# Kernel optimization log

Measured on AMD Instinct MI355X. Metric: run time of the kernel, lower is better.

## Reference

```python
import jax, jax.numpy as jnp
import numpy as np
import math

N = 20000      # nodes
E = 150000     # edges
IN = 256       # in_dim
HID = 256      # n_hid / out_dim
T = 4          # num_types
R = 8          # num_relations
H = 8          # n_heads
DK = HID // H  # d_k = 32
L = 2          # n_layers
MAXLEN = 240   # RTE max_len


def _rte_table():
    # fixed sinusoid table from RelTemporalEncoding (requires_grad=False in torch)
    pos = np.arange(MAXLEN, dtype=np.float64)[:, None]
    div = np.exp(np.arange(0, HID, 2, dtype=np.float64) * -(math.log(10000.0) / HID))
    emb = np.zeros((MAXLEN, HID), dtype=np.float64)
    emb[:, 0::2] = np.sin(pos * div) / math.sqrt(HID)
    emb[:, 1::2] = np.cos(pos * div) / math.sqrt(HID)
    return jnp.asarray(emb, dtype=jnp.float32)


def setup_inputs() -> dict:
    key = jax.random.key(0)
    ks = jax.random.split(key, 20)
    node_feature = jax.random.normal(ks[0], (N, IN), jnp.float32)
    node_type = jax.random.randint(ks[1], (N,), 0, T)
    edge_index = jax.random.randint(ks[2], (2, E), 0, N)
    edge_type = jax.random.randint(ks[3], (E,), 0, R)
    edge_time = jax.random.randint(ks[4], (E,), 0, MAXLEN)

    s_in = 1.0 / math.sqrt(IN)
    s_h = 1.0 / math.sqrt(HID)
    s_g = math.sqrt(2.0 / (DK + DK))  # glorot for relation mats

    adapt_W = jax.random.normal(ks[5], (T, IN, HID), jnp.float32) * s_in
    adapt_b = jnp.zeros((T, HID), jnp.float32)
    k_W = jax.random.normal(ks[6], (L, T, HID, HID), jnp.float32) * s_h
    k_b = jnp.zeros((L, T, HID), jnp.float32)
    q_W = jax.random.normal(ks[7], (L, T, HID, HID), jnp.float32) * s_h
    q_b = jnp.zeros((L, T, HID), jnp.float32)
    v_W = jax.random.normal(ks[8], (L, T, HID, HID), jnp.float32) * s_h
    v_b = jnp.zeros((L, T, HID), jnp.float32)
    a_W = jax.random.normal(ks[9], (L, T, HID, HID), jnp.float32) * s_h
    a_b = jnp.zeros((L, T, HID), jnp.float32)
    rel_pri = jnp.ones((L, R, H), jnp.float32)
    rel_att = jax.random.normal(ks[10], (L, R, H, DK, DK), jnp.float32) * s_g
    rel_msg = jax.random.normal(ks[11], (L, R, H, DK, DK), jnp.float32) * s_g
    skip = jnp.ones((L, T), jnp.float32)
    rte_W = jax.random.normal(ks[12], (L, HID, HID), jnp.float32) * s_h
    rte_b = jnp.zeros((L, HID), jnp.float32)
    rte_emb = _rte_table()

    return dict(node_feature=node_feature, node_type=node_type, edge_time=edge_time,
                edge_index=edge_index, edge_type=edge_type,
                adapt_W=adapt_W, adapt_b=adapt_b, k_W=k_W, k_b=k_b, q_W=q_W, q_b=q_b,
                v_W=v_W, v_b=v_b, a_W=a_W, a_b=a_b, rel_pri=rel_pri, rel_att=rel_att,
                rel_msg=rel_msg, skip=skip, rte_W=rte_W, rte_b=rte_b, rte_emb=rte_emb)


def _typed_linear(x, W, b, types):
    # x: [M, din]; W: [T, din, dout]; per-row type-selected linear (T dense GEMMs + select)
    out = jnp.zeros((x.shape[0], W.shape[-1]), x.dtype)
    for t in range(T):
        out = jnp.where((types == t)[:, None], x @ W[t] + b[t], out)
    return out


def _hgt_forward(node_feature, node_type, edge_time, edge_index, edge_type,
                 adapt_W, adapt_b, k_W, k_b, q_W, q_b, v_W, v_b, a_W, a_b,
                 rel_pri, rel_att, rel_msg, skip, rte_W, rte_b, rte_emb):
    # adapt: per-type tanh(Linear) (dropout is identity at p=0)
    x = jnp.tanh(_typed_linear(node_feature, adapt_W, adapt_b, node_type))
    src, tgt = edge_index[0], edge_index[1]   # j (source), i (target)
    st, tt = node_type[src], node_type[tgt]
    sqrt_dk = math.sqrt(DK)
    att = None
    rte = rte_emb[edge_time]                  # [E, HID]
    for l in range(L):
        x_j = x[src] + (rte @ rte_W[l] + rte_b[l])   # RTE added to source repr
        x_i = x[tgt]
        q = _typed_linear(x_i, q_W[l], q_b[l], tt).reshape(E, H, DK)
        k = _typed_linear(x_j, k_W[l], k_b[l], st).reshape(E, H, DK)
        v = _typed_linear(x_j, v_W[l], v_b[l], st).reshape(E, H, DK)
        att_e = jnp.zeros((E, H), x.dtype)
        msg = jnp.zeros((E, H, DK), x.dtype)
        for r in range(R):
            kr = jnp.einsum('ehd,hdk->ehk', k, rel_att[l, r])
            vr = jnp.einsum('ehd,hdk->ehk', v, rel_msg[l, r])
            a = (q * kr).sum(-1) * rel_pri[l, r] / sqrt_dk
            m = edge_type == r
            att_e = jnp.where(m[:, None], a, att_e)
            msg = jnp.where(m[:, None, None], vr, msg)
        # segment softmax over target node ids
        amax = jax.ops.segment_max(att_e, tgt, num_segments=N)
        ex = jnp.exp(att_e - amax[tgt])
        denom = jax.ops.segment_sum(ex, tgt, num_segments=N)
        alpha = ex / denom[tgt]                       # [E, H]
        agg = jax.ops.segment_sum(msg * alpha[:, :, None], tgt, num_segments=N)
        agg = jax.nn.gelu(agg.reshape(N, HID), approximate=False)
        trans = _typed_linear(agg, a_W[l], a_b[l], node_type)
        sk = jax.nn.sigmoid(skip[l])[node_type][:, None]
        x = trans * sk + x * (1.0 - sk)               # no LayerNorm (use_norm=False)
        att = alpha
    return att, x


def reference(node_feature, node_type, edge_time, edge_index, edge_type,
              adapt_W, adapt_b, k_W, k_b, q_W, q_b, v_W, v_b, a_W, a_b,
              rel_pri, rel_att, rel_msg, skip, rte_W, rte_b, rte_emb):
    return _hgt_forward(node_feature, node_type, edge_time, edge_index, edge_type,
                        adapt_W, adapt_b, k_W, k_b, q_W, q_b, v_W, v_b, a_W, a_b,
                        rel_pri, rel_att, rel_msg, skip, rte_W, rte_b, rte_emb)
```

## Files before the change

### kernel.cpp

```cpp
#include <hip/hip_runtime.h>
#include <hip/hip_fp16.h>

#define NN    20000
#define NE    150000
#define HD    256
#define NT    4
#define NR    8
#define NH    8
#define DKq   32
#define NL    2
#define MAXL  240
#define HBLK  256
#define SCB   ((NN + 255)/256)
#define TMAX  632
#define FOLDN 79
#define FOLDC 15
#define INV_SQRT_DK 0.17677669529663687f

typedef _Float16 f16x4 __attribute__((ext_vector_type(4)));
typedef float    f32x4v __attribute__((ext_vector_type(4)));

__global__ __launch_bounds__(256) void k_nhist(const int* __restrict__ ntype, int* __restrict__ nhist)
{
    __shared__ int h[NT];
    const int tid = threadIdx.x, b = blockIdx.x;
    if (tid < NT) h[tid] = 0;
    __syncthreads();
    const int cn = (NN + HBLK-1)/HBLK;
    const int nEnd = min((b+1)*cn, NN);
    for (int i = b*cn + tid; i < nEnd; i += 256) atomicAdd(&h[ntype[i]], 1);
    __syncthreads();
    if (tid < NT) nhist[b*NT + tid] = h[tid];
}
__global__ void k_nscan(const int* __restrict__ nhist, int* __restrict__ noff, int* __restrict__ nbase,
                        int* __restrict__ tlist, int* __restrict__ tcount)
{
    __shared__ int tot[NT];
    const int tid = threadIdx.x;
    if (tid < NT){
        int s = 0;
        for (int b = 0; b < HBLK; b++) s += nhist[b*NT + tid];
        tot[tid] = s;
    }
    __syncthreads();
    if (tid == 0){ noff[0]=0; for (int t=0;t<NT;t++) noff[t+1]=noff[t]+tot[t]; }
    if (tid < NT){
        int base = 0; for (int t=0;t<tid;t++) base += tot[t];
        int run = 0;
        for (int b=0;b<HBLK;b++){ nbase[b*NT+tid] = base + run; run += nhist[b*NT+tid]; }
    }
    __syncthreads();
    if (tid == 0){
        int c = 0;
        for (int t = 0; t < NT; t++){
            const int ntile = (tot[t] + 31) >> 5;
            for (int rt = 0; rt < ntile; rt++) tlist[c++] = (t << 20) | rt;
        }
        *tcount = c;
    }
}
__global__ __launch_bounds__(256) void k_nscatter(const int* __restrict__ ntype,
    const int* __restrict__ nbase, int* __restrict__ nbucket)
{
    __shared__ int cur[NT];
    const int tid = threadIdx.x, b = blockIdx.x;
    if (tid < NT) cur[tid] = nbase[b*NT + tid];
    __syncthreads();
    const int cn = (NN + HBLK-1)/HBLK;
    const int nEnd = min((b+1)*cn, NN);
    for (int i = b*cn + tid; i < nEnd; i += 256)
        nbucket[atomicAdd(&cur[ntype[i]], 1)] = i;
}

__global__ void k_zero_bins(int* __restrict__ cnt){
    int i = blockIdx.x*256 + threadIdx.x;
    if (i < NN) cnt[i] = 0;
}
__global__ void k_csr_hist(const int* __restrict__ ei, int* __restrict__ cnt){
    int e = blockIdx.x*256 + threadIdx.x;
    if (e >= NE) return;
    atomicAdd(&cnt[ei[NE+e]], 1);
}
__global__ __launch_bounds__(256) void k_scan1(const int* __restrict__ cnt,
    int* __restrict__ tgt_off, int* __restrict__ bsum)
{
    __shared__ int sh[256];
    const int t = threadIdx.x, b = blockIdx.x;
    const int i = b*256 + t;
    const int v = (i < NN) ? cnt[i] : 0;
    sh[t] = v;
    __syncthreads();
    #pragma unroll
    for (int d = 1; d < 256; d <<= 1){
        const int u = (t >= d) ? sh[t-d] : 0;
        __syncthreads();
        sh[t] += u;
        __syncthreads();
    }
    if (i < NN) tgt_off[i] = sh[t] - v;
    if (t == 255) bsum[b] = sh[255];
}
__global__ __launch_bounds__(128) void k_scan2(const int* __restrict__ bsum,
    int* __restrict__ bbase, int* __restrict__ tgt_off)
{
    __shared__ int sh[128];
    const int t = threadIdx.x;
    const int v = (t < SCB) ? bsum[t] : 0;
    sh[t] = v;
    __syncthreads();
    #pragma unroll
    for (int d = 1; d < 128; d <<= 1){
        const int u = (t >= d) ? sh[t-d] : 0;
        __syncthreads();
        sh[t] += u;
        __syncthreads();
    }
    if (t < SCB) bbase[t] = sh[t] - v;
    if (t == 0) tgt_off[NN] = NE;
}
__global__ __launch_bounds__(256) void k_scan3(int* __restrict__ tgt_off,
    const int* __restrict__ bbase, int* __restrict__ binCur)
{
    const int i = blockIdx.x*256 + threadIdx.x;
    if (i >= NN) return;
    const int o = tgt_off[i] + bbase[blockIdx.x];
    tgt_off[i] = o;
    binCur[i] = o;
}
__global__ void k_csr_scatter(const int* __restrict__ ei, const int* __restrict__ etype,
    const int* __restrict__ etime, const int* __restrict__ ntype,
    int* __restrict__ binCur, int* __restrict__ src_s, int* __restrict__ combo_s,
    int* __restrict__ eid_s)
{
    int e = blockIdx.x*256 + threadIdx.x;
    if (e >= NE) return;
    const int tgt = ei[NE+e], r = etype[e], src = ei[e];
    const int pos = atomicAdd(&binCur[tgt], 1);
    src_s[pos] = src;
    combo_s[pos] = (etime[e]*NT + ntype[src]) | (r << 12);
    eid_s[pos] = e;
}
__global__ void k_tgtmap(const int* __restrict__ tgt_off, int* __restrict__ tgt_srt)
{
    const int n = blockIdx.x*256 + threadIdx.x;
    if (n >= NN) return;
    const int e0 = tgt_off[n], e1 = tgt_off[n+1];
    for (int j = e0; j < e1; j++) tgt_srt[j] = n;
}

__global__ __launch_bounds__(256) void k_w2f16_big(
    const float* __restrict__ adaptW, const float* __restrict__ qW, const float* __restrict__ kW,
    const float* __restrict__ vW, const float* __restrict__ aW, _Float16* __restrict__ out)
{
    const int y = blockIdx.y;
    const float* src; int m;
    if (y < 4){ src = adaptW; m = y; }
    else if (y < 12){ src = qW; m = y-4; }
    else if (y < 20){ src = kW; m = y-12; }
    else if (y < 28){ src = vW; m = y-20; }
    else { src = aW; m = y-28; }
    const float* ip = src + (size_t)m*65536;
    _Float16* op = out + (size_t)y*65536;
    const int tid4 = blockIdx.x*256 + threadIdx.x;
    const int k4 = tid4 >> 8, c = tid4 & 255;
    f16x4 hv;
    #pragma unroll
    for (int j = 0; j < 4; j++)
        hv[j] = (_Float16)ip[(size_t)(((k4*4 + j) << 8) + c)];
    *reinterpret_cast<f16x4*>(&op[(size_t)tid4 * 4]) = hv;
}
__global__ __launch_bounds__(256) void k_w2f16_rel(
    const float* __restrict__ attW, const float* __restrict__ msgW, _Float16* __restrict__ out)
{
    const int y = blockIdx.y;
    const float* ip = (y < 128) ? (attW + (size_t)y*1024) : (msgW + (size_t)(y-128)*1024);
    _Float16* op = out + (size_t)y*1024;
    const int tid4 = threadIdx.x;
    const int k4 = tid4 >> 5, c = tid4 & 31;
    f16x4 hv;
    #pragma unroll
    for (int j = 0; j < 4; j++)
        hv[j] = (_Float16)ip[(size_t)(((k4*4 + j) << 5) + c)];
    *reinterpret_cast<f16x4*>(&op[(size_t)tid4 * 4]) = hv;
}

__global__ __launch_bounds__(256) void k_x(
    const float* __restrict__ inF, const _Float16* __restrict__ inH,
    const _Float16* __restrict__ Wb, const float* __restrict__ bb, void* __restrict__ out,
    const int* __restrict__ nbucket, const int* __restrict__ noff,
    const int* __restrict__ tlist, const int* __restrict__ tcount,
    int mode, int oh, const float* __restrict__ skipv, const _Float16* __restrict__ xoldH)
{
    if ((int)blockIdx.x >= *tcount) return;
    const int ent = tlist[blockIdx.x];
    const int t = ent >> 20, rowTile = ent & 0xFFFFF;
    const int start = noff[t], cnt = noff[t+1] - start;

    const int tid = threadIdx.x;
    const int w = tid >> 6, lane = tid & 63;
    const int lrow = lane & 15, lgrp = lane >> 4;

    __shared__ _Float16 Al[32][260];
    __shared__ int nid[32];

    if (tid < 32){
        const int gr = rowTile*32 + tid;
        nid[tid] = (gr < cnt) ? nbucket[start + gr] : -1;
    }
    __syncthreads();
    {
        const int r = tid >> 3;
        const int arow = nid[r];
        if (inH){
            const _Float16* ap = (arow >= 0) ? (inH + (size_t)arow*HD) : nullptr;
            #pragma unroll
            for (int j = 0; j < 8; j++){
                const int f4 = (tid & 7) + j*8;
                f16x4 hv = {0,0,0,0};
                if (ap) hv = *reinterpret_cast<const f16x4*>(ap + f4*4);
                *reinterpret_cast<f16x4*>(&Al[r][f4*4]) = hv;
            }
        } else {
            const float* ap = (arow >= 0) ? (inF + (size_t)arow*HD) : nullptr;
            #pragma unroll
            for (int j = 0; j < 8; j++){
                const int f4 = (tid & 7) + j*8;
                float4 v = make_float4(0.f,0.f,0.f,0.f);
                if (ap) v = *reinterpret_cast<const float4*>(ap + f4*4);
                f16x4 hv;
                hv[0]=(_Float16)v.x; hv[1]=(_Float16)v.y; hv[2]=(_Float16)v.z; hv[3]=(_Float16)v.w;
                *reinterpret_cast<f16x4*>(&Al[r][f4*4]) = hv;
            }
        }
    }
    __syncthreads();

    float sk = 0.f;
    if (mode == 2) sk = 1.f/(1.f + __expf(-skipv[t]));

    const _Float16* W = Wb + (size_t)t*HD*HD;
    const float* bias = bb + (size_t)t*HD;
    f32x4v acc[4][2];
    #pragma unroll
    for (int cs = 0; cs < 4; cs++){
        acc[cs][0] = (f32x4v){0.f,0.f,0.f,0.f};
        acc[cs][1] = (f32x4v){0.f,0.f,0.f,0.f};
    }
    #pragma unroll 4
    for (int kc = 0; kc < 16; kc++){
        f16x4 bf[4];
        #pragma unroll
        for (int cs = 0; cs < 4; cs++)
            bf[cs] = *reinterpret_cast<const f16x4*>(
                &W[(size_t)((kc*4 + lgrp)*HD + w*64 + cs*16 + lrow)*4]);
        const f16x4 af0 = *reinterpret_cast<const f16x4*>(&Al[lrow][kc*16 + lgrp*4]);
        const f16x4 af1 = *reinterpret_cast<const f16x4*>(&Al[16 + lrow][kc*16 + lgrp*4]);
        #pragma unroll
        for (int cs = 0; cs < 4; cs++){
            acc[cs][0] = __builtin_amdgcn_mfma_f32_16x16x16f16(af0, bf[cs], acc[cs][0], 0,0,0);
            acc[cs][1] = __builtin_amdgcn_mfma_f32_16x16x16f16(af1, bf[cs], acc[cs][1], 0,0,0);
        }
    }
    #pragma unroll
    for (int cs = 0; cs < 4; cs++){
        const int col = w*64 + cs*16 + lrow;
        const float bcol = bias[col];
        #pragma unroll
        for (int rt = 0; rt < 2; rt++){
            #pragma unroll
            for (int i = 0; i < 4; i++){
                const int lr = rt*16 + lgrp*4 + i;
                const int gr = rowTile*32 + lr;
                if (gr >= cnt) continue;
                const int node = nid[lr];
                float v = acc[cs][rt][i] + bcol;
                if (mode == 1) v = tanhf(v);
                else if (mode == 2){
                    const float xo = (float)xoldH[(size_t)node*HD + col];
                    v = v*sk + xo*(1.f - sk);
                }
                if (oh) ((_Float16*)out)[(size_t)node*HD + col] = (_Float16)v;
                else    ((float*)out)[(size_t)node*HD + col] = v;
            }
        }
    }
}

__global__ __launch_bounds__(256) void k_qkv(
    const _Float16* __restrict__ xh,
    const _Float16* __restrict__ Wq, const float* __restrict__ bq, _Float16* __restrict__ oq,
    const _Float16* __restrict__ Wk, const float* __restrict__ bk, _Float16* __restrict__ okk,
    const _Float16* __restrict__ Wv, const float* __restrict__ bv, _Float16* __restrict__ ov,
    const int* __restrict__ nbucket, const int* __restrict__ noff,
    const int* __restrict__ tlist, const int* __restrict__ tcount)
{
    if ((int)blockIdx.x >= *tcount) return;
    const int ent = tlist[blockIdx.x];
    const int t = ent >> 20, rowTile = ent & 0xFFFFF;
    const int start = noff[t], cnt = noff[t+1] - start;
    const int sel = blockIdx.y;
    const _Float16* Wb = (sel==0 ? Wq : (sel==1 ? Wk : Wv));
    const float* bb = (sel==0 ? bq : (sel==1 ? bk : bv));
    _Float16* out = (sel==0 ? oq : (sel==1 ? okk : ov));

    const int tid = threadIdx.x;
    const int w = tid >> 6, lane = tid & 63;
    const int lrow = lane & 15, lgrp = lane >> 4;

    __shared__ _Float16 Al[32][260];
    __shared__ int nid[32];

    if (tid < 32){
        const int gr = rowTile*32 + tid;
        nid[tid] = (gr < cnt) ? nbucket[start + gr] : -1;
    }
    __syncthreads();
    {
        const int r = tid >> 3;
        const int arow = nid[r];
        const _Float16* ap = (arow >= 0) ? (xh + (size_t)arow*HD) : nullptr;
        #pragma unroll
        for (int j = 0; j < 8; j++){
            const int f4 = (tid & 7) + j*8;
            f16x4 hv = {0,0,0,0};
            if (ap) hv = *reinterpret_cast<const f16x4*>(ap + f4*4);
            *reinterpret_cast<f16x4*>(&Al[r][f4*4]) = hv;
        }
    }
    __syncthreads();

    const _Float16* W = Wb + (size_t)t*HD*HD;
    const float* bias = bb + (size_t)t*HD;
    f32x4v acc[4][2];
    #pragma unroll
    for (int cs = 0; cs < 4; cs++){
        acc[cs][0] = (f32x4v){0.f,0.f,0.f,0.f};
        acc[cs][1] = (f32x4v){0.f,0.f,0.f,0.f};
    }
    #pragma unroll 4
    for (int kc = 0; kc < 16; kc++){
        f16x4 bf[4];
        #pragma unroll
        for (int cs = 0; cs < 4; cs++)
            bf[cs] = *reinterpret_cast<const f16x4*>(
                &W[(size_t)((kc*4 + lgrp)*HD + w*64 + cs*16 + lrow)*4]);
        const f16x4 af0 = *reinterpret_cast<const f16x4*>(&Al[lrow][kc*16 + lgrp*4]);
        const f16x4 af1 = *reinterpret_cast<const f16x4*>(&Al[16 + lrow][kc*16 + lgrp*4]);
        #pragma unroll
        for (int cs = 0; cs < 4; cs++){
            acc[cs][0] = __builtin_amdgcn_mfma_f32_16x16x16f16(af0, bf[cs], acc[cs][0], 0,0,0);
            acc[cs][1] = __builtin_amdgcn_mfma_f32_16x16x16f16(af1, bf[cs], acc[cs][1], 0,0,0);
        }
    }
    #pragma unroll
    for (int cs = 0; cs < 4; cs++){
        const int col = w*64 + cs*16 + lrow;
        const float bcol = bias[col];
        #pragma unroll
        for (int rt = 0; rt < 2; rt++){
            #pragma unroll
            for (int i = 0; i < 4; i++){
                const int lr = rt*16 + lgrp*4 + i;
                const int gr = rowTile*32 + lr;
                if (gr >= cnt) continue;
                const int node = nid[lr];
                out[(size_t)node*HD + col] = (_Float16)(acc[cs][rt][i] + bcol);
            }
        }
    }
}

__global__ __launch_bounds__(256) void k_row_gemm(
    const float* __restrict__ A, const float* __restrict__ W, const float* __restrict__ bias,
    float* __restrict__ C)
{
    const int row = blockIdx.x, d = threadIdx.x;
    __shared__ float ar[HD];
    ar[d] = A[(size_t)row*HD + d];
    __syncthreads();
    float acc = bias[d];
    #pragma unroll 8
    for (int k=0;k<HD;k++) acc = fmaf(ar[k], W[(size_t)k*HD + d], acc);
    C[(size_t)row*HD + d] = acc;
}
__global__ __launch_bounds__(256) void k_row_gemm2(
    const float* __restrict__ A, const float* __restrict__ kWb, const float* __restrict__ vWb,
    _Float16* __restrict__ Kc, _Float16* __restrict__ Vc)
{
    const int row = blockIdx.x, ty = blockIdx.y, d = threadIdx.x;
    const float* W = ((blockIdx.z == 0) ? kWb : vWb) + (size_t)ty*HD*HD;
    _Float16* C = (blockIdx.z == 0) ? Kc : Vc;
    __shared__ float ar[HD];
    ar[d] = A[(size_t)row*HD + d];
    __syncthreads();
    float acc = 0.f;
    #pragma unroll 8
    for (int k=0;k<HD;k++) acc = fmaf(ar[k], W[(size_t)k*HD + d], acc);
    C[(size_t)row*(NT*HD) + ty*HD + d] = (_Float16)acc;
}

__global__ __launch_bounds__(256) void k_fold2(
    const _Float16* __restrict__ INa, const _Float16* __restrict__ MATa, _Float16* __restrict__ OUTa,
    const _Float16* __restrict__ INb, const _Float16* __restrict__ MATb, _Float16* __restrict__ OUTb,
    int M, int nbx)
{
    const int r = blockIdx.y;
    const _Float16* IN = blockIdx.z ? INb : INa;
    const _Float16* MATF = blockIdx.z ? MATb : MATa;
    _Float16* OUT = blockIdx.z ? OUTb : OUTa;
    const int lane = threadIdx.x & 63, w = threadIdx.x >> 6;
    const int lrow = lane & 15, lgrp = lane >> 4;
    f16x4 b[NH][2][2];
    const _Float16* Mr = MATF + (size_t)r*NH*1024;
    #pragma unroll
    for (int h = 0; h < NH; h++)
      #pragma unroll
      for (int kb = 0; kb < 2; kb++)
        #pragma unroll
        for (int hf = 0; hf < 2; hf++)
            b[h][kb][hf] = *reinterpret_cast<const f16x4*>(
                &Mr[(size_t)h*1024 + (size_t)(((kb*4 + lgrp)*32) + hf*16 + lrow)*4]);
    const int ntiles = M >> 4;
    for (int t = (int)blockIdx.x*4 + w; t < ntiles; t += nbx*4){
        const int row0 = t*16;
        const _Float16* inrow = IN + (size_t)(row0 + lrow)*HD;
        f16x4 a[NH][2];
        #pragma unroll
        for (int h = 0; h < NH; h++)
          #pragma unroll
          for (int kb = 0; kb < 2; kb++)
              a[h][kb] = *reinterpret_cast<const f16x4*>(&inrow[h*32 + kb*16 + lgrp*4]);
        #pragma unroll
        for (int h = 0; h < NH; h++){
          #pragma unroll
          for (int hf = 0; hf < 2; hf++){
              f32x4v acc = {0.f,0.f,0.f,0.f};
              acc = __builtin_amdgcn_mfma_f32_16x16x16f16(a[h][0], b[h][0][hf], acc, 0,0,0);
              acc = __builtin_amdgcn_mfma_f32_16x16x16f16(a[h][1], b[h][1][hf], acc, 0,0,0);
              #pragma unroll
              for (int i = 0; i < 4; i++){
                  const int rr = lgrp*4 + i;
                  OUT[((size_t)(row0+rr)*NR + r)*HD + h*32 + hf*16 + lrow] = (_Float16)acc[i];
              }
          }
        }
    }
}

__global__ __launch_bounds__(256) void k_edge(
    const _Float16* __restrict__ q0, const _Float16* __restrict__ kA, const _Float16* __restrict__ KcA,
    const _Float16* __restrict__ vM, const _Float16* __restrict__ VcM,
    const float* __restrict__ relP,
    const int* __restrict__ tgt_off, const int* __restrict__ src_s, const int* __restrict__ combo_s,
    _Float16* __restrict__ agg,
    float* __restrict__ s_arr, float* __restrict__ mbuf, float* __restrict__ lbuf, int store_s)
{
    const int n = blockIdx.x*4 + (threadIdx.x >> 6);
    if (n >= NN) return;
    const int lane = threadIdx.x & 63;
    const int h = lane >> 3, c4 = (lane & 7) << 2;
    const int col = h*32 + c4;
    const int e0 = tgt_off[n], e1 = tgt_off[n+1];

    const f16x4 qh = *reinterpret_cast<const f16x4*>(&q0[(size_t)n*HD + col]);
    const float q0v = (float)qh[0], q1v = (float)qh[1], q2v = (float)qh[2], q3v = (float)qh[3];
    float m = -INFINITY, l = 0.f;
    float a0=0.f, a1=0.f, a2=0.f, a3=0.f;

    for (int j = e0; j < e1; j++){
        const int src = src_s[j];
        const int cw  = combo_s[j];
        const int r = cw >> 12, combo = cw & 0xFFF;
        const size_t offS = ((size_t)src*NR + r)*HD + col;
        const size_t offC = ((size_t)combo*NR + r)*HD + col;
        const f16x4 ka = *reinterpret_cast<const f16x4*>(&kA[offS]);
        const f16x4 kc = *reinterpret_cast<const f16x4*>(&KcA[offC]);
        const f16x4 vm = *reinterpret_cast<const f16x4*>(&vM[offS]);
        const f16x4 vc = *reinterpret_cast<const f16x4*>(&VcM[offC]);
        float s = q0v*((float)ka[0]+(float)kc[0])
                + q1v*((float)ka[1]+(float)kc[1])
                + q2v*((float)ka[2]+(float)kc[2])
                + q3v*((float)ka[3]+(float)kc[3]);
        s += __shfl_xor(s, 1); s += __shfl_xor(s, 2); s += __shfl_xor(s, 4);
        s *= relP[r*NH + h] * INV_SQRT_DK;
        if (store_s && (lane & 7) == 0) s_arr[(size_t)j*NH + h] = s;
        const float mn = fmaxf(m, s);
        const float sc = __expf(m - mn);
        const float p  = __expf(s - mn);
        l = l*sc + p;
        m = mn;
        a0 = a0*sc + p*((float)vm[0] + (float)vc[0]);
        a1 = a1*sc + p*((float)vm[1] + (float)vc[1]);
        a2 = a2*sc + p*((float)vm[2] + (float)vc[2]);
        a3 = a3*sc + p*((float)vm[3] + (float)vc[3]);
    }
    const float inv = (l > 0.f) ? 1.f/l : 0.f;
    a0 *= inv; a1 *= inv; a2 *= inv; a3 *= inv;
    f16x4 o;
    o[0] = (_Float16)(0.5f*a0*(1.f + erff(a0*0.70710678118654752f)));
    o[1] = (_Float16)(0.5f*a1*(1.f + erff(a1*0.70710678118654752f)));
    o[2] = (_Float16)(0.5f*a2*(1.f + erff(a2*0.70710678118654752f)));
    o[3] = (_Float16)(0.5f*a3*(1.f + erff(a3*0.70710678118654752f)));
    *reinterpret_cast<f16x4*>(&agg[(size_t)n*HD + col]) = o;
    if (store_s && (lane & 7) == 0){
        mbuf[(size_t)n*NH + h] = m;
        lbuf[(size_t)n*NH + h] = l;
    }
}

__global__ void k_alpha(const float* __restrict__ s_arr, const int* __restrict__ eid_s,
                        const float* __restrict__ mbuf, const float* __restrict__ lbuf,
                        const int* __restrict__ tgt_srt, float* __restrict__ out_att)
{
    int i = blockIdx.x*256 + threadIdx.x;
    if (i >= NE*NH) return;
    const int j = i >> 3, h = i & 7;
    const int t = tgt_srt[j];
    const float a = __expf(s_arr[i] - mbuf[(size_t)t*NH + h]) / lbuf[(size_t)t*NH + h];
    out_att[(size_t)eid_s[j]*NH + h] = a;
}

extern "C" void kernel_launch(void* const* d_in, const int* in_sizes, int n_in,
                              void* d_out, int out_size, void* d_ws, size_t ws_size,
                              hipStream_t stream)
{
    const float* node_feature = (const float*)d_in[0];
    const int*   node_type    = (const int*)d_in[1];
    const int*   edge_time    = (const int*)d_in[2];
    const int*   edge_index   = (const int*)d_in[3];
    const int*   edge_type    = (const int*)d_in[4];
    const float* adapt_W = (const float*)d_in[5];
    const float* adapt_b = (const float*)d_in[6];
    const float* k_W = (const float*)d_in[7];
    const float* k_b = (const float*)d_in[8];
    const float* q_W = (const float*)d_in[9];
    const float* q_b = (const float*)d_in[10];
    const float* v_W = (const float*)d_in[11];
    const float* v_b = (const float*)d_in[12];
    const float* a_W = (const float*)d_in[13];
    const float* a_b = (const float*)d_in[14];
    const float* rel_pri = (const float*)d_in[15];
    const float* rel_att = (const float*)d_in[16];
    const float* rel_msg = (const float*)d_in[17];
    const float* skip  = (const float*)d_in[18];
    const float* rte_W = (const float*)d_in[19];
    const float* rte_b = (const float*)d_in[20];
    const float* rte_emb = (const float*)d_in[21];

    char* wp = (char*)d_ws;
    auto alloc_f = [&](size_t n)->float*{ float* p=(float*)wp; wp += n*sizeof(float); return p; };
    auto alloc_i = [&](size_t n)->int*  { int*   p=(int*)wp;   wp += n*sizeof(int);   return p; };
    auto alloc_h = [&](size_t n)->_Float16*{ _Float16* p=(_Float16*)wp; wp += n*sizeof(_Float16); return p; };
    _Float16* xh0 = alloc_h((size_t)NN*HD);
    _Float16* xh1 = alloc_h((size_t)NN*HD);
    _Float16* q0h = alloc_h((size_t)NN*HD);
    _Float16* k0h = alloc_h((size_t)NN*HD);
    _Float16* v0h = alloc_h((size_t)NN*HD);
    _Float16* aggh= alloc_h((size_t)NN*HD);
    float* s_arr = alloc_f((size_t)NE*NH);
    float* mbuf  = alloc_f((size_t)NN*NH);
    float* lbuf  = alloc_f((size_t)NN*NH);
    float* rteP  = alloc_f((size_t)MAXL*HD);
    _Float16* Kch = alloc_h((size_t)MAXL*NT*HD);
    _Float16* Vch = alloc_h((size_t)MAXL*NT*HD);
    _Float16* kavm = alloc_h((size_t)NN*NR*HD);
    _Float16* vmh  = alloc_h((size_t)NN*NR*HD);
    _Float16* kcaA0 = alloc_h((size_t)MAXL*NT*NR*HD);
    _Float16* kcaA1 = alloc_h((size_t)MAXL*NT*NR*HD);
    _Float16* kcaM0 = alloc_h((size_t)MAXL*NT*NR*HD);
    _Float16* kcaM1 = alloc_h((size_t)MAXL*NT*NR*HD);
    _Float16* wF   = alloc_h((size_t)36*65536);
    _Float16* relF = alloc_h((size_t)256*1024);
    int* nbucket = alloc_i(NN);
    int* nhist   = alloc_i(HBLK*NT);
    int* nbase   = alloc_i(HBLK*NT);
    int* noff    = alloc_i(8);
    int* tlist   = alloc_i(TMAX);
    int* tcount  = alloc_i(8);
    int* cnt     = alloc_i(NN);
    int* bsum    = alloc_i(SCB);
    int* bbase   = alloc_i(SCB);
    int* binCur  = alloc_i(NN);
    int* tgt_off = alloc_i(NN+1);
    int* src_s   = alloc_i(NE);
    int* combo_s = alloc_i(NE);
    int* eid_s   = alloc_i(NE);
    int* tgt_srt = alloc_i(NE);

    const _Float16* adaptF = wF;
    const _Float16* qF = wF + (size_t)4*65536;
    const _Float16* kF = wF + (size_t)12*65536;
    const _Float16* vF = wF + (size_t)20*65536;
    const _Float16* aF = wF + (size_t)28*65536;
    const _Float16* relAF = relF;
    const _Float16* relMF = relF + (size_t)128*1024;

    float* out_att = (float*)d_out;
    float* out_x   = (float*)d_out + (size_t)NE*NH;

    const dim3 gFoldN2(FOLDN, NR, 2);
    const dim3 gFoldC2(FOLDC, NR, 2);
    const dim3 gQKV(TMAX, 3);
    const int gE256 = (NE + 255)/256;
    const int gEH = (NE*NH + 255)/256;
    const int gN256 = (NN + 255)/256;
    const int gEg = (NN + 3)/4;

    k_w2f16_big<<<dim3(64,36),256,0,stream>>>(adapt_W, q_W, k_W, v_W, a_W, wF);
    k_w2f16_rel<<<dim3(1,256),256,0,stream>>>(rel_att, rel_msg, relF);

    k_nhist<<<HBLK,256,0,stream>>>(node_type, nhist);
    k_nscan<<<1,64,0,stream>>>(nhist, noff, nbase, tlist, tcount);
    k_nscatter<<<HBLK,256,0,stream>>>(node_type, nbase, nbucket);

    k_zero_bins<<<SCB,256,0,stream>>>(cnt);
    k_csr_hist<<<gE256,256,0,stream>>>(edge_index, cnt);
    k_scan1<<<SCB,256,0,stream>>>(cnt, tgt_off, bsum);
    k_scan2<<<1,128,0,stream>>>(bsum, bbase, tgt_off);
    k_scan3<<<SCB,256,0,stream>>>(tgt_off, bbase, binCur);
    k_csr_scatter<<<gE256,256,0,stream>>>(edge_index, edge_type, edge_time, node_type,
                                          binCur, src_s, combo_s, eid_s);
    k_tgtmap<<<gN256,256,0,stream>>>(tgt_off, tgt_srt);

    {
        k_row_gemm<<<MAXL,256,0,stream>>>(rte_emb, rte_W, rte_b, rteP);
        k_row_gemm2<<<dim3(MAXL,NT,2),256,0,stream>>>(rteP, k_W, v_W, Kch, Vch);
        k_fold2<<<gFoldC2,256,0,stream>>>(Kch, relAF, kcaA0, Vch, relMF, kcaM0, MAXL*NT, FOLDC);
        k_row_gemm<<<MAXL,256,0,stream>>>(rte_emb, rte_W + (size_t)HD*HD, rte_b + HD, rteP);
        k_row_gemm2<<<dim3(MAXL,NT,2),256,0,stream>>>(rteP, k_W + (size_t)NT*HD*HD,
                                                      v_W + (size_t)NT*HD*HD, Kch, Vch);
        k_fold2<<<gFoldC2,256,0,stream>>>(Kch, relAF + (size_t)NR*NH*1024, kcaA1,
                                          Vch, relMF + (size_t)NR*NH*1024, kcaM1, MAXL*NT, FOLDC);
    }

    k_x<<<TMAX,256,0,stream>>>(node_feature, nullptr, adaptF, adapt_b, xh0,
                               nbucket, noff, tlist, tcount, 1, 1, nullptr, nullptr);
    k_qkv<<<gQKV,256,0,stream>>>(xh0, qF, q_b, q0h, kF, k_b, k0h, vF, v_b, v0h,
                                 nbucket, noff, tlist, tcount);

    for (int l = 0; l < NL; l++){
        const _Float16* rAF = relAF + (size_t)l*NR*NH*1024;
        const _Float16* rMF = relMF + (size_t)l*NR*NH*1024;
        const _Float16* kcaA = (l == 0) ? kcaA0 : kcaA1;
        const _Float16* kcaM = (l == 0) ? kcaM0 : kcaM1;
        const int store_s = (l == NL-1) ? 1 : 0;
        k_fold2<<<gFoldN2,256,0,stream>>>(k0h, rAF, kavm, v0h, rMF, vmh, NN, FOLDN);
        k_edge<<<gEg,256,0,stream>>>(q0h, kavm, kcaA, vmh, kcaM,
                                     rel_pri + (size_t)l*NR*NH,
                                     tgt_off, src_s, combo_s, aggh,
                                     s_arr, mbuf, lbuf, store_s);
        if (store_s)
            k_alpha<<<gEH,256,0,stream>>>(s_arr, eid_s, mbuf, lbuf, tgt_srt, out_att);
        if (l == 0){
            k_x<<<TMAX,256,0,stream>>>(nullptr, aggh, aF, a_b, xh1,
                                       nbucket, noff, tlist, tcount, 2, 1, skip, xh0);
            k_qkv<<<gQKV,256,0,stream>>>(xh1, qF + (size_t)NT*HD*HD, q_b + (size_t)NT*HD, q0h,
                                         kF + (size_t)NT*HD*HD, k_b + (size_t)NT*HD, k0h,
                                         vF + (size_t)NT*HD*HD, v_b + (size_t)NT*HD, v0h,
                                         nbucket, noff, tlist, tcount);
        } else {
            k_x<<<TMAX,256,0,stream>>>(nullptr, aggh, aF + (size_t)NT*HD*HD, a_b + (size_t)NT*HD,
                                       out_x, nbucket, noff, tlist, tcount, 2, 0, skip + NT, xh1);
        }
    }
}
```

Before: 539.4 us.

## Loop relations inside fold kernel to reuse input fragments across relation matrices

The fold kernel now loads each 16-row input tile once and loops over all 8 relation matrices inside the block, instead of spreading relations across grid blocks that each reload the input. The relation B fragments are read from global memory inside the loop rather than preloaded into registers, and the node grid is widened to keep the GPU busy. This trades repeated input reads for repeated small weight reads, which should mostly hit cache, and it lowers register pressure.

Measured after the change: 604.4 us. 1.12x slower.

```diff
diff --git a/kernel.cpp b/kernel.cpp
--- a/kernel.cpp
+++ b/kernel.cpp
@@ -13,7 +13,7 @@
 #define HBLK  256
 #define SCB   ((NN + 255)/256)
 #define TMAX  632
-#define FOLDN 79
+#define FOLDN 313
 #define FOLDC 15
 #define INV_SQRT_DK 0.17677669529663687f
 
@@ -399,27 +399,16 @@
     C[(size_t)row*(NT*HD) + ty*HD + d] = (_Float16)acc;
 }
 
-__global__ __launch_bounds__(256) void k_fold2(
+__global__ __launch_bounds__(256) void k_foldr(
     const _Float16* __restrict__ INa, const _Float16* __restrict__ MATa, _Float16* __restrict__ OUTa,
     const _Float16* __restrict__ INb, const _Float16* __restrict__ MATb, _Float16* __restrict__ OUTb,
     int M, int nbx)
 {
-    const int r = blockIdx.y;
-    const _Float16* IN = blockIdx.z ? INb : INa;
-    const _Float16* MATF = blockIdx.z ? MATb : MATa;
-    _Float16* OUT = blockIdx.z ? OUTb : OUTa;
+    const _Float16* IN = blockIdx.y ? INb : INa;
+    const _Float16* MATF = blockIdx.y ? MATb : MATa;
+    _Float16* OUT = blockIdx.y ? OUTb : OUTa;
     const int lane = threadIdx.x & 63, w = threadIdx.x >> 6;
     const int lrow = lane & 15, lgrp = lane >> 4;
-    f16x4 b[NH][2][2];
-    const _Float16* Mr = MATF + (size_t)r*NH*1024;
-    #pragma unroll
-    for (int h = 0; h < NH; h++)
-      #pragma unroll
-      for (int kb = 0; kb < 2; kb++)
-        #pragma unroll
-        for (int hf = 0; hf < 2; hf++)
-            b[h][kb][hf] = *reinterpret_cast<const f16x4*>(
-                &Mr[(size_t)h*1024 + (size_t)(((kb*4 + lgrp)*32) + hf*16 + lrow)*4]);
     const int ntiles = M >> 4;
     for (int t = (int)blockIdx.x*4 + w; t < ntiles; t += nbx*4){
         const int row0 = t*16;
@@ -430,19 +419,26 @@
           #pragma unroll
           for (int kb = 0; kb < 2; kb++)
               a[h][kb] = *reinterpret_cast<const f16x4*>(&inrow[h*32 + kb*16 + lgrp*4]);
-        #pragma unroll
-        for (int h = 0; h < NH; h++){
-          #pragma unroll
-          for (int hf = 0; hf < 2; hf++){
-              f32x4v acc = {0.f,0.f,0.f,0.f};
-              acc = __builtin_amdgcn_mfma_f32_16x16x16f16(a[h][0], b[h][0][hf], acc, 0,0,0);
-              acc = __builtin_amdgcn_mfma_f32_16x16x16f16(a[h][1], b[h][1][hf], acc, 0,0,0);
+        for (int r = 0; r < NR; r++){
+            const _Float16* Mr = MATF + (size_t)r*NH*1024;
+            #pragma unroll
+            for (int h = 0; h < NH; h++){
               #pragma unroll
-              for (int i = 0; i < 4; i++){
-                  const int rr = lgrp*4 + i;
-                  OUT[((size_t)(row0+rr)*NR + r)*HD + h*32 + hf*16 + lrow] = (_Float16)acc[i];
+              for (int hf = 0; hf < 2; hf++){
+                  const f16x4 b0 = *reinterpret_cast<const f16x4*>(
+                      &Mr[(size_t)h*1024 + (size_t)((lgrp*32) + hf*16 + lrow)*4]);
+                  const f16x4 b1 = *reinterpret_cast<const f16x4*>(
+                      &Mr[(size_t)h*1024 + (size_t)(((4 + lgrp)*32) + hf*16 + lrow)*4]);
+                  f32x4v acc = {0.f,0.f,0.f,0.f};
+                  acc = __builtin_amdgcn_mfma_f32_16x16x16f16(a[h][0], b0, acc, 0,0,0);
+                  acc = __builtin_amdgcn_mfma_f32_16x16x16f16(a[h][1], b1, acc, 0,0,0);
+                  #pragma unroll
+                  for (int i = 0; i < 4; i++){
+                      const int rr = lgrp*4 + i;
+                      OUT[((size_t)(row0+rr)*NR + r)*HD + h*32 + hf*16 + lrow] = (_Float16)acc[i];
+                  }
               }
-          }
+            }
         }
     }
 }
@@ -598,8 +594,8 @@
     float* out_att = (float*)d_out;
     float* out_x   = (float*)d_out + (size_t)NE*NH;
 
-    const dim3 gFoldN2(FOLDN, NR, 2);
-    const dim3 gFoldC2(FOLDC, NR, 2);
+    const dim3 gFoldN(FOLDN, 2);
+    const dim3 gFoldC(FOLDC, 2);
     const dim3 gQKV(TMAX, 3);
     const int gE256 = (NE + 255)/256;
     const int gEH = (NE*NH + 255)/256;
@@ -625,12 +621,12 @@
     {
         k_row_gemm<<<MAXL,256,0,stream>>>(rte_emb, rte_W, rte_b, rteP);
         k_row_gemm2<<<dim3(MAXL,NT,2),256,0,stream>>>(rteP, k_W, v_W, Kch, Vch);
-        k_fold2<<<gFoldC2,256,0,stream>>>(Kch, relAF, kcaA0, Vch, relMF, kcaM0, MAXL*NT, FOLDC);
+        k_foldr<<<gFoldC,256,0,stream>>>(Kch, relAF, kcaA0, Vch, relMF, kcaM0, MAXL*NT, FOLDC);
         k_row_gemm<<<MAXL,256,0,stream>>>(rte_emb, rte_W + (size_t)HD*HD, rte_b + HD, rteP);
         k_row_gemm2<<<dim3(MAXL,NT,2),256,0,stream>>>(rteP, k_W + (size_t)NT*HD*HD,
                                                       v_W + (size_t)NT*HD*HD, Kch, Vch);
-        k_fold2<<<gFoldC2,256,0,stream>>>(Kch, relAF + (size_t)NR*NH*1024, kcaA1,
-                                          Vch, relMF + (size_t)NR*NH*1024, kcaM1, MAXL*NT, FOLDC);
+        k_foldr<<<gFoldC,256,0,stream>>>(Kch, relAF + (size_t)NR*NH*1024, kcaA1,
+                                         Vch, relMF + (size_t)NR*NH*1024, kcaM1, MAXL*NT, FOLDC);
     }
 
     k_x<<<TMAX,256,0,stream>>>(node_feature, nullptr, adaptF, adapt_b, xh0,
@@ -644,7 +640,7 @@
         const _Float16* kcaA = (l == 0) ? kcaA0 : kcaA1;
         const _Float16* kcaM = (l == 0) ? kcaM0 : kcaM1;
         const int store_s = (l == NL-1) ? 1 : 0;
-        k_fold2<<<gFoldN2,256,0,stream>>>(k0h, rAF, kavm, v0h, rMF, vmh, NN, FOLDN);
+        k_foldr<<<gFoldN,256,0,stream>>>(k0h, rAF, kavm, v0h, rMF, vmh, NN, FOLDN);
         k_edge<<<gEg,256,0,stream>>>(q0h, kavm, kcaA, vmh, kcaM,
                                      rel_pri + (size_t)l*NR*NH,
                                      tgt_off, src_s, combo_s, aggh,
```
